# Kernel tuning notes

Measured on AMD Instinct MI355X. Metric: run time of the kernel, lower is better.

## Reference

```python
import jax, jax.numpy as jnp
import numpy as np

D_MODEL = 512
N_HEADS = 8
B, S = 4, 1024
REL_HIDDEN = 64


def setup_inputs() -> dict:
    key = jax.random.key(0)
    ks = jax.random.split(key, 16)

    def g(k, shape, scale=0.02):
        return jax.random.normal(k, shape, dtype=jnp.float32) * scale

    x = jax.random.normal(ks[0], (B, S, D_MODEL), dtype=jnp.float32)
    freqs = jax.random.uniform(ks[1], (B, S, 1), dtype=jnp.float32)
    return {
        "x": x,
        "freqs": freqs,
        "Wq": g(ks[2], (D_MODEL, D_MODEL)), "bq": g(ks[3], (D_MODEL,)),
        "Wk": g(ks[4], (D_MODEL, D_MODEL)), "bk": g(ks[5], (D_MODEL,)),
        "Wv": g(ks[6], (D_MODEL, D_MODEL)), "bv": g(ks[7], (D_MODEL,)),
        "Wo": g(ks[8], (D_MODEL, D_MODEL)), "bo": g(ks[9], (D_MODEL,)),
        "W1": g(ks[10], (2, REL_HIDDEN)), "b1": g(ks[11], (REL_HIDDEN,)),
        "W2": g(ks[12], (REL_HIDDEN, N_HEADS)), "b2": g(ks[13], (N_HEADS,)),
    }


def reference(x, freqs, Wq, bq, Wk, bk, Wv, bv, Wo, bo, W1, b1, W2, b2):
    b, s, d = x.shape
    h = N_HEADS
    dh = d // h

    def proj(W, bias):  # (b,s,d) -> (b,h,s,dh)
        return (x @ W + bias).reshape(b, s, h, dh).transpose(0, 2, 1, 3)

    Q = proj(Wq, bq)
    K = proj(Wk, bk)
    V = proj(Wv, bv)

    scores = jnp.einsum('bhid,bhjd->bhij', Q, K) / jnp.sqrt(jnp.float32(dh))

    # per-pair relative-frequency features: (b,s,s,2)
    eps = 1e-6
    fd = freqs[:, :, None, :] - freqs[:, None, :, :]
    fr = jnp.log((freqs[:, :, None, :] + eps) / (freqs[:, None, :, :] + eps))
    rel = jnp.concatenate([fd, fr], axis=-1)

    # MLP bias -> (b,s,s,h) -> (b,h,s,s)
    bias = jax.nn.relu(rel @ W1 + b1) @ W2 + b2
    scores = scores + jnp.transpose(bias, (0, 3, 1, 2))

    attn = jax.nn.softmax(scores, axis=-1)
    ctx = jnp.einsum('bhij,bhjd->bhid', attn, V)
    ctx = ctx.transpose(0, 2, 1, 3).reshape(b, s, d)
    return ctx @ Wo + bo
```

## Files before the change

### kernel.cpp

```cpp
#include <hip/hip_runtime.h>
#include <hip/hip_bf16.h>
#include <cstdint>

#define BATCH   4
#define SEQ     1024
#define DM      512
#define NH      8
#define DH      64
#define RH      64

typedef float f32x4 __attribute__((ext_vector_type(4)));
typedef __bf16 bf16x8 __attribute__((ext_vector_type(8)));

#define QB_OFF    (0)
#define KB_OFF    (4  << 20)
#define VT_OFF    (8  << 20)
#define XB_OFF    (12 << 20)
#define WT_OFF    (16 << 20)
#define WOT_OFF   (18 << 20)
#define W2T_OFF   (19 << 20)
#define AW_OFF    (20 << 20)
#define CW_OFF    (21 << 20)
#define CTXB_OFF  (22 << 20)
#define BIAS_OFF  (32 << 20)

__global__ __launch_bounds__(256) void prologue(
    const float* __restrict__ x,
    const float* __restrict__ Wq, const float* __restrict__ Wk,
    const float* __restrict__ Wv, const float* __restrict__ Wo,
    const float* __restrict__ freqs, const float* __restrict__ W1,
    const float* __restrict__ b1, const float* __restrict__ W2,
    __bf16* __restrict__ xb, __bf16* __restrict__ Wt,
    __bf16* __restrict__ Wot, float* __restrict__ Aw,
    float* __restrict__ Cw, __bf16* __restrict__ W2t)
{
    const int t = threadIdx.x;
    const int id = blockIdx.x;
    __shared__ __align__(16) float Ts[64][65];

    if (id < 1024) {
        const size_t i = ((size_t)id * 256 + t) * 8;
        const float4 a = *(const float4*)&x[i];
        const float4 b = *(const float4*)&x[i + 4];
        bf16x8 o;
        o[0] = (__bf16)a.x; o[1] = (__bf16)a.y; o[2] = (__bf16)a.z; o[3] = (__bf16)a.w;
        o[4] = (__bf16)b.x; o[5] = (__bf16)b.y; o[6] = (__bf16)b.z; o[7] = (__bf16)b.w;
        *(bf16x8*)&xb[i] = o;
    } else if (id < 1280) {
        const int lin = id - 1024;
        const int z   = lin >> 6;
        const int rem = lin & 63;
        const int k0  = (rem >> 3) * 64;
        const int n0  = (rem & 7) * 64;
        const float* __restrict__ src = (z == 0) ? Wq : (z == 1) ? Wk
                                       : (z == 2) ? Wv : Wo;
        __bf16* __restrict__ dst = (z < 3) ? (Wt + (size_t)(z * 512 + n0) * 512)
                                           : (Wot + (size_t)n0 * 512);
        #pragma unroll
        for (int i = 0; i < 4; ++i) {
            const int iid = t + i * 256;
            const int row = iid >> 4, c4 = (iid & 15) * 4;
            const float4 v = *(const float4*)&src[(size_t)(k0 + row) * DM + n0 + c4];
            Ts[row][c4 + 0] = v.x; Ts[row][c4 + 1] = v.y;
            Ts[row][c4 + 2] = v.z; Ts[row][c4 + 3] = v.w;
        }
        __syncthreads();
        #pragma unroll
        for (int i = 0; i < 2; ++i) {
            const int iid = t + i * 256;
            const int rn = iid >> 3, ck = (iid & 7) * 8;
            bf16x8 o;
            #pragma unroll
            for (int j = 0; j < 8; ++j) o[j] = (__bf16)Ts[ck + j][rn];
            *(bf16x8*)&dst[(size_t)rn * 512 + k0 + ck] = o;
        }
    } else {
        const int lin = id - 1280;
        const int row = lin * 4 + (t >> 6);
        const int k = t & 63;
        const float f = freqs[row];
        const float L = logf(f + 1e-6f);
        const float base = f * W1[k] + L * W1[RH + k];
        Aw[(size_t)row * RH + k] = base + b1[k];
        Cw[(size_t)row * RH + k] = -base;
        if (row < 16)
            W2t[row * 64 + k] = (row < NH) ? (__bf16)W2[k * NH + row] : (__bf16)0.f;
    }
}

__global__ __launch_bounds__(256) void mid_fused(
    const __bf16* __restrict__ xb, const __bf16* __restrict__ Wt,
    const float* __restrict__ bq, const float* __restrict__ bk,
    const float* __restrict__ bv,
    __bf16* __restrict__ Qb, __bf16* __restrict__ Kb, __bf16* __restrict__ Vtb,
    const float* __restrict__ Aw, const float* __restrict__ Cw,
    const __bf16* __restrict__ W2t, __bf16* __restrict__ biasb)
{
    const int t = threadIdx.x;
    __shared__ __align__(16) char smem[36864];

    if (blockIdx.x < 384) {
        const int wave = t >> 6, lane = t & 63;
        const int wm = wave >> 1, wn = wave & 1;
        const int r = lane & 15, kc = lane >> 4, q4 = kc * 4;
        const int lin = blockIdx.x;
        const int swz = (lin & 7) * 48 + (lin >> 3);
        const int m0 = (swz / 12) * 128;
        const int n0 = (swz % 12) * 128;
        const int sec = n0 >> 9;
        const int nn = n0 & 511;

        __bf16* __restrict__ As = (__bf16*)smem;
        __bf16* __restrict__ Bs = (__bf16*)(smem + 18432);

        f32x4 acc[4][4];
        #pragma unroll
        for (int i = 0; i < 4; ++i)
            #pragma unroll
            for (int j = 0; j < 4; ++j) acc[i][j] = {0.f, 0.f, 0.f, 0.f};

        const int srow = t >> 3, sck = (t & 7) * 8;
        const __bf16* __restrict__ Ag = xb + (size_t)(m0 + srow) * 512 + sck;
        const __bf16* __restrict__ Bg = Wt + (size_t)(n0 + srow) * 512 + sck;

        for (int k0 = 0; k0 < 512; k0 += 64) {
            bf16x8 ra[4], rb[4];
            #pragma unroll
            for (int i = 0; i < 4; ++i) {
                ra[i] = *(const bf16x8*)(Ag + (size_t)i * 32 * 512 + k0);
                rb[i] = *(const bf16x8*)(Bg + (size_t)i * 32 * 512 + k0);
            }
            __syncthreads();
            #pragma unroll
            for (int i = 0; i < 4; ++i) {
                *(bf16x8*)&As[(srow + i * 32) * 72 + sck] = ra[i];
                *(bf16x8*)&Bs[(srow + i * 32) * 72 + sck] = rb[i];
            }
            __syncthreads();
            #pragma unroll
            for (int ks = 0; ks < 2; ++ks) {
                bf16x8 af[4], bf[4];
                #pragma unroll
                for (int mf = 0; mf < 4; ++mf)
                    af[mf] = *(const bf16x8*)&As[(wm * 64 + mf * 16 + r) * 72 + ks * 32 + kc * 8];
                #pragma unroll
                for (int nf = 0; nf < 4; ++nf)
                    bf[nf] = *(const bf16x8*)&Bs[(wn * 64 + nf * 16 + r) * 72 + ks * 32 + kc * 8];
                #pragma unroll
                for (int mf = 0; mf < 4; ++mf)
                    #pragma unroll
                    for (int nf = 0; nf < 4; ++nf)
                        acc[mf][nf] = __builtin_amdgcn_mfma_f32_16x16x32_bf16(
                            af[mf], bf[nf], acc[mf][nf], 0, 0, 0);
            }
        }

        const float* __restrict__ bias = (sec == 0) ? bq : (sec == 1) ? bk : bv;
        __syncthreads();
        __bf16* __restrict__ Ls = (__bf16*)smem;
        if (sec < 2) {
            #pragma unroll
            for (int mf = 0; mf < 4; ++mf)
                #pragma unroll
                for (int nf = 0; nf < 4; ++nf) {
                    const int n_l = wn * 64 + nf * 16 + r;
                    const float bb = bias[nn + n_l];
                    #pragma unroll
                    for (int rr = 0; rr < 4; ++rr)
                        Ls[(wm * 64 + mf * 16 + q4 + rr) * 136 + n_l] =
                            (__bf16)(acc[mf][nf][rr] + bb);
                }
        } else {
            #pragma unroll
            for (int mf = 0; mf < 4; ++mf)
                #pragma unroll
                for (int nf = 0; nf < 4; ++nf) {
                    const int n_l = wn * 64 + nf * 16 + r;
                    const float bb = bias[nn + n_l];
                    #pragma unroll
                    for (int rr = 0; rr < 4; ++rr)
                        Ls[n_l * 136 + (wm * 64 + mf * 16 + q4 + rr)] =
                            (__bf16)(acc[mf][nf][rr] + bb);
                }
        }
        __syncthreads();

        const int b = m0 >> 10, sbase = m0 & 1023;
        if (sec < 2) {
            __bf16* __restrict__ dst = sec ? Kb : Qb;
            #pragma unroll
            for (int i = 0; i < 8; ++i) {
                const int id = t + i * 256;
                const int row = id >> 4, nc = (id & 15) * 8;
                const bf16x8 v = *(const bf16x8*)&Ls[row * 136 + nc];
                const int ng = nn + nc, h = ng >> 6, c = ng & 63;
                *(bf16x8*)&dst[((size_t)(b * NH + h) * SEQ + sbase + row) * DH + c] = v;
            }
        } else {
            #pragma unroll
            for (int i = 0; i < 8; ++i) {
                const int id = t + i * 256;
                const int nrow = id >> 4, mc = (id & 15) * 8;
                const bf16x8 v = *(const bf16x8*)&Ls[nrow * 136 + mc];
                const int ng = nn + nrow, h = ng >> 6, c = ng & 63;
                *(bf16x8*)&Vtb[((size_t)(b * NH + h) * DH + c) * SEQ + sbase + mc] = v;
            }
        }
    } else {
        const int wave = t >> 6, lane = t & 63;
        const int il = lane & 15, kc = lane >> 4;
        const int id2 = blockIdx.x - 384;
        const int b   = id2 >> 8;
        const int rem = id2 & 255;
        const int i0  = (rem >> 3) * 32;
        const int j0  = (rem & 7) * 128;

        float* __restrict__ Cs = (float*)smem;

        {
            const int jr = t >> 1, half = (t & 1) * 32;
            const float* __restrict__ src = &Cw[((size_t)b * SEQ + j0 + jr) * RH + half];
            #pragma unroll
            for (int q = 0; q < 8; ++q)
                *(float4*)&Cs[jr * 68 + half + q * 4] = *(const float4*)(src + q * 4);
        }

        const bf16x8 w2f0 = *(const bf16x8*)&W2t[il * 64 + kc * 8];
        const bf16x8 w2f1 = *(const bf16x8*)&W2t[il * 64 + 32 + kc * 8];
        __syncthreads();

        #pragma unroll
        for (int ih = 0; ih < 2; ++ih) {
            const float* __restrict__ ap =
                &Aw[((size_t)b * SEQ + i0 + ih * 16 + il) * RH];
            const float4 a0 = *(const float4*)(ap + kc * 8);
            const float4 a1 = *(const float4*)(ap + kc * 8 + 4);
            const float4 a2 = *(const float4*)(ap + 32 + kc * 8);
            const float4 a3 = *(const float4*)(ap + 32 + kc * 8 + 4);

            #pragma unroll
            for (int jb = 0; jb < 4; ++jb) {
                f32x4 accJ[8];
                #pragma unroll
                for (int jj = 0; jj < 8; ++jj) {
                    const float* __restrict__ cp =
                        &Cs[(wave * 32 + jb * 8 + jj) * 68 + kc * 8];
                    const float4 c0 = *(const float4*)(cp);
                    const float4 c1 = *(const float4*)(cp + 4);
                    const float4 c2 = *(const float4*)(cp + 32);
                    const float4 c3 = *(const float4*)(cp + 36);
                    bf16x8 hb0, hb1;
                    hb0[0] = (__bf16)fmaxf(a0.x + c0.x, 0.f);
                    hb0[1] = (__bf16)fmaxf(a0.y + c0.y, 0.f);
                    hb0[2] = (__bf16)fmaxf(a0.z + c0.z, 0.f);
                    hb0[3] = (__bf16)fmaxf(a0.w + c0.w, 0.f);
                    hb0[4] = (__bf16)fmaxf(a1.x + c1.x, 0.f);
                    hb0[5] = (__bf16)fmaxf(a1.y + c1.y, 0.f);
                    hb0[6] = (__bf16)fmaxf(a1.z + c1.z, 0.f);
                    hb0[7] = (__bf16)fmaxf(a1.w + c1.w, 0.f);
                    hb1[0] = (__bf16)fmaxf(a2.x + c2.x, 0.f);
                    hb1[1] = (__bf16)fmaxf(a2.y + c2.y, 0.f);
                    hb1[2] = (__bf16)fmaxf(a2.z + c2.z, 0.f);
                    hb1[3] = (__bf16)fmaxf(a2.w + c2.w, 0.f);
                    hb1[4] = (__bf16)fmaxf(a3.x + c3.x, 0.f);
                    hb1[5] = (__bf16)fmaxf(a3.y + c3.y, 0.f);
                    hb1[6] = (__bf16)fmaxf(a3.z + c3.z, 0.f);
                    hb1[7] = (__bf16)fmaxf(a3.w + c3.w, 0.f);
                    f32x4 acc = {0.f, 0.f, 0.f, 0.f};
                    acc = __builtin_amdgcn_mfma_f32_16x16x32_bf16(hb0, w2f0, acc, 0, 0, 0);
                    acc = __builtin_amdgcn_mfma_f32_16x16x32_bf16(hb1, w2f1, acc, 0, 0, 0);
                    accJ[jj] = acc;
                }
                if (il < 8) {
                    #pragma unroll
                    for (int rr = 0; rr < 4; ++rr) {
                        bf16x8 pv;
                        #pragma unroll
                        for (int jj = 0; jj < 8; ++jj)
                            pv[jj] = (__bf16)accJ[jj][rr];
                        *(bf16x8*)&biasb[(((size_t)b * NH + il) * SEQ
                                          + i0 + ih * 16 + kc * 4 + rr) * SEQ
                                         + j0 + wave * 32 + jb * 8] = pv;
                    }
                }
            }
        }
    }
}

#define PSTR 1032

__global__ __launch_bounds__(512) void attn_mfma(
    const __bf16* __restrict__ Qb, const __bf16* __restrict__ Kb,
    const __bf16* __restrict__ Vtb, const __bf16* __restrict__ biasb,
    __bf16* __restrict__ ctxb)
{
    const int t = threadIdx.x;
    const int wave = t >> 6, lane = t & 63;
    const int r = lane & 15, kc = lane >> 4;
    const int blk = (blockIdx.x & 7) * 256 + (blockIdx.x >> 3);
    const int it = blk & 63;
    const int h  = (blk >> 6) & 7;
    const int b  = blk >> 9;
    const int s0 = it * 16;
    const int bh = b * NH + h;

    __shared__ __align__(16) __bf16 Pb[16 * PSTR];
    __shared__ __align__(16) float part[1088];
    __shared__ float red[8][16];
    __shared__ float invl[16];

    uint32_t brg[4][8];
    {
        const uint16_t* __restrict__ bb = (const uint16_t*)biasb
            + ((size_t)bh * SEQ + s0 + kc * 4) * SEQ + wave * 128 + r;
        #pragma unroll
        for (int rr = 0; rr < 4; ++rr)
            #pragma unroll
            for (int jt = 0; jt < 8; ++jt)
                brg[rr][jt] = bb[(size_t)rr * SEQ + jt * 16];
    }

    f32x4 sc[8];
    {
        const __bf16* __restrict__ Qp = Qb + ((size_t)bh * SEQ + s0) * DH;
        const __bf16* __restrict__ Kp = Kb + ((size_t)bh * SEQ + wave * 128) * DH;
        const bf16x8 qa0 = *(const bf16x8*)(Qp + r * DH + kc * 8);
        const bf16x8 qa1 = *(const bf16x8*)(Qp + r * DH + 32 + kc * 8);
        __builtin_amdgcn_s_setprio(1);
        #pragma unroll
        for (int jt = 0; jt < 8; ++jt) {
            const bf16x8 kb0 = *(const bf16x8*)(Kp + (size_t)(jt * 16 + r) * DH + kc * 8);
            const bf16x8 kb1 = *(const bf16x8*)(Kp + (size_t)(jt * 16 + r) * DH + 32 + kc * 8);
            f32x4 a = {0.f, 0.f, 0.f, 0.f};
            a = __builtin_amdgcn_mfma_f32_16x16x32_bf16(qa0, kb0, a, 0, 0, 0);
            a = __builtin_amdgcn_mfma_f32_16x16x32_bf16(qa1, kb1, a, 0, 0, 0);
            sc[jt] = a;
        }
        __builtin_amdgcn_s_setprio(0);
    }

    float psum[4] = {0.f, 0.f, 0.f, 0.f};
    #pragma unroll
    for (int jt = 0; jt < 8; ++jt) {
        #pragma unroll
        for (int rr = 0; rr < 4; ++rr) {
            const float s = fmaf(sc[jt][rr], 0.125f,
                                 __uint_as_float(brg[rr][jt] << 16));
            const float p = __expf(fminf(s, 30.f));
            sc[jt][rr] = p;
            psum[rr] += p;
        }
    }
    #pragma unroll
    for (int mask = 8; mask >= 1; mask >>= 1)
        #pragma unroll
        for (int rr = 0; rr < 4; ++rr)
            psum[rr] += __shfl_xor(psum[rr], mask);
    if (r == 0) {
        #pragma unroll
        for (int rr = 0; rr < 4; ++rr) red[wave][kc * 4 + rr] = psum[rr];
    }
    #pragma unroll
    for (int jt = 0; jt < 8; ++jt)
        #pragma unroll
        for (int rr = 0; rr < 4; ++rr)
            Pb[(kc * 4 + rr) * PSTR + wave * 128 + jt * 16 + r] = (__bf16)sc[jt][rr];
    __syncthreads();

    if (t < 16) {
        float l = 0.f;
        #pragma unroll
        for (int w = 0; w < 8; ++w) l += red[w][t];
        invl[t] = 1.0f / l;
    }

    {
        const int ct = wave & 3, kh = wave >> 2;
        const __bf16* __restrict__ Vp =
            Vtb + ((size_t)bh * DH + ct * 16 + r) * SEQ + kh * 512;
        f32x4 acc = {0.f, 0.f, 0.f, 0.f};
        __builtin_amdgcn_s_setprio(1);
        #pragma unroll 4
        for (int jt = 0; jt < 16; ++jt) {
            const bf16x8 pa = *(const bf16x8*)&Pb[r * PSTR + kh * 512 + jt * 32 + kc * 8];
            const bf16x8 vb = *(const bf16x8*)(Vp + jt * 32 + kc * 8);
            acc = __builtin_amdgcn_mfma_f32_16x16x32_bf16(pa, vb, acc, 0, 0, 0);
        }
        __builtin_amdgcn_s_setprio(0);
        if (kh == 1) {
            #pragma unroll
            for (int rr = 0; rr < 4; ++rr)
                part[ct * 272 + (kc * 4 + rr) * 17 + r] = acc[rr];
        }
        __syncthreads();
        if (kh == 0) {
            #pragma unroll
            for (int rr = 0; rr < 4; ++rr) {
                const int row = kc * 4 + rr;
                const float v = (acc[rr] + part[ct * 272 + row * 17 + r]) * invl[row];
                ctxb[((size_t)(b * SEQ) + s0 + row) * DM + h * DH + ct * 16 + r] = (__bf16)v;
            }
        }
    }
}

__global__ __launch_bounds__(256) void gemm_out_mfma(
    const __bf16* __restrict__ ctxb, const __bf16* __restrict__ Wot,
    const float* __restrict__ bo, float* __restrict__ out)
{
    const int t = threadIdx.x;
    const int wave = t >> 6, lane = t & 63;
    const int wm = wave >> 1, wn = wave & 1;
    const int r = lane & 15, kc = lane >> 4, q4 = kc * 4;
    const int lin = blockIdx.y * 4 + blockIdx.x;
    const int swz = (lin & 7) * 16 + (lin >> 3);
    const int m0 = (swz / 4) * 128;
    const int n0 = (swz % 4) * 128;

    __shared__ __align__(16) char smem[36864];
    __bf16* __restrict__ As = (__bf16*)smem;
    __bf16* __restrict__ Bs = (__bf16*)(smem + 18432);

    f32x4 acc[4][4];
    #pragma unroll
    for (int i = 0; i < 4; ++i)
        #pragma unroll
        for (int j = 0; j < 4; ++j) acc[i][j] = {0.f, 0.f, 0.f, 0.f};

    const int srow = t >> 3, sck = (t & 7) * 8;
    const __bf16* __restrict__ Ag = ctxb + (size_t)(m0 + srow) * 512 + sck;
    const __bf16* __restrict__ Bg = Wot + (size_t)(n0 + srow) * 512 + sck;

    for (int k0 = 0; k0 < 512; k0 += 64) {
        bf16x8 ra[4], rb[4];
        #pragma unroll
        for (int i = 0; i < 4; ++i) {
            ra[i] = *(const bf16x8*)(Ag + (size_t)i * 32 * 512 + k0);
            rb[i] = *(const bf16x8*)(Bg + (size_t)i * 32 * 512 + k0);
        }
        __syncthreads();
        #pragma unroll
        for (int i = 0; i < 4; ++i) {
            *(bf16x8*)&As[(srow + i * 32) * 72 + sck] = ra[i];
            *(bf16x8*)&Bs[(srow + i * 32) * 72 + sck] = rb[i];
        }
        __syncthreads();
        #pragma unroll
        for (int ks = 0; ks < 2; ++ks) {
            bf16x8 af[4], bf[4];
            #pragma unroll
            for (int mf = 0; mf < 4; ++mf)
                af[mf] = *(const bf16x8*)&As[(wm * 64 + mf * 16 + r) * 72 + ks * 32 + kc * 8];
            #pragma unroll
            for (int nf = 0; nf < 4; ++nf)
                bf[nf] = *(const bf16x8*)&Bs[(wn * 64 + nf * 16 + r) * 72 + ks * 32 + kc * 8];
            #pragma unroll
            for (int mf = 0; mf < 4; ++mf)
                #pragma unroll
                for (int nf = 0; nf < 4; ++nf)
                    acc[mf][nf] = __builtin_amdgcn_mfma_f32_16x16x32_bf16(
                        af[mf], bf[nf], acc[mf][nf], 0, 0, 0);
        }
    }

    #pragma unroll
    for (int mf = 0; mf < 4; ++mf)
        #pragma unroll
        for (int nf = 0; nf < 4; ++nf) {
            const int n_l = wn * 64 + nf * 16 + r;
            const float bb = bo[n0 + n_l];
            #pragma unroll
            for (int rr = 0; rr < 4; ++rr)
                out[(size_t)(m0 + wm * 64 + mf * 16 + q4 + rr) * DM + n0 + n_l] =
                    acc[mf][nf][rr] + bb;
        }
}

extern "C" void kernel_launch(void* const* d_in, const int* in_sizes, int n_in,
                              void* d_out, int out_size, void* d_ws, size_t ws_size,
                              hipStream_t stream)
{
    const float* x     = (const float*)d_in[0];
    const float* freqs = (const float*)d_in[1];
    const float* Wq    = (const float*)d_in[2];
    const float* bq    = (const float*)d_in[3];
    const float* Wk    = (const float*)d_in[4];
    const float* bk    = (const float*)d_in[5];
    const float* Wv    = (const float*)d_in[6];
    const float* bv    = (const float*)d_in[7];
    const float* Wo    = (const float*)d_in[8];
    const float* bo    = (const float*)d_in[9];
    const float* W1    = (const float*)d_in[10];
    const float* b1    = (const float*)d_in[11];
    const float* W2    = (const float*)d_in[12];

    char* wsb = (char*)d_ws;
    __bf16* Qb    = (__bf16*)(wsb + QB_OFF);
    __bf16* Kb    = (__bf16*)(wsb + KB_OFF);
    __bf16* Vtb   = (__bf16*)(wsb + VT_OFF);
    __bf16* xb    = (__bf16*)(wsb + XB_OFF);
    __bf16* Wt    = (__bf16*)(wsb + WT_OFF);
    __bf16* Wot   = (__bf16*)(wsb + WOT_OFF);
    __bf16* W2t   = (__bf16*)(wsb + W2T_OFF);
    float*  Aw    = (float*)(wsb + AW_OFF);
    float*  Cw    = (float*)(wsb + CW_OFF);
    __bf16* ctxb  = (__bf16*)(wsb + CTXB_OFF);
    __bf16* biasb = (__bf16*)(wsb + BIAS_OFF);
    float* out = (float*)d_out;

    prologue<<<dim3(2304), 256, 0, stream>>>(
        x, Wq, Wk, Wv, Wo, freqs, W1, b1, W2, xb, Wt, Wot, Aw, Cw, W2t);
    mid_fused<<<dim3(1408), 256, 0, stream>>>(
        xb, Wt, bq, bk, bv, Qb, Kb, Vtb, Aw, Cw, W2t, biasb);
    attn_mfma<<<dim3(2048), 512, 0, stream>>>(Qb, Kb, Vtb, biasb, ctxb);
    gemm_out_mfma<<<dim3(4, 32), 256, 0, stream>>>(ctxb, Wot, bo, out);
}
```

Baseline: 207.7 us.

## Fuse prologue conversions into consumer kernels, dropping the prologue launch

```diff
diff --git a/kernel.cpp b/kernel.cpp
--- a/kernel.cpp
+++ b/kernel.cpp
@@ -15,86 +15,19 @@
 #define QB_OFF    (0)
 #define KB_OFF    (4  << 20)
 #define VT_OFF    (8  << 20)
-#define XB_OFF    (12 << 20)
-#define WT_OFF    (16 << 20)
-#define WOT_OFF   (18 << 20)
-#define W2T_OFF   (19 << 20)
-#define AW_OFF    (20 << 20)
-#define CW_OFF    (21 << 20)
-#define CTXB_OFF  (22 << 20)
+#define CTXB_OFF  (12 << 20)
 #define BIAS_OFF  (32 << 20)
 
-__global__ __launch_bounds__(256) void prologue(
+__global__ __launch_bounds__(256) void mid2(
     const float* __restrict__ x,
     const float* __restrict__ Wq, const float* __restrict__ Wk,
-    const float* __restrict__ Wv, const float* __restrict__ Wo,
+    const float* __restrict__ Wv,
+    const float* __restrict__ bq, const float* __restrict__ bk,
+    const float* __restrict__ bv,
     const float* __restrict__ freqs, const float* __restrict__ W1,
     const float* __restrict__ b1, const float* __restrict__ W2,
-    __bf16* __restrict__ xb, __bf16* __restrict__ Wt,
-    __bf16* __restrict__ Wot, float* __restrict__ Aw,
-    float* __restrict__ Cw, __bf16* __restrict__ W2t)
-{
-    const int t = threadIdx.x;
-    const int id = blockIdx.x;
-    __shared__ __align__(16) float Ts[64][65];
-
-    if (id < 1024) {
-        const size_t i = ((size_t)id * 256 + t) * 8;
-        const float4 a = *(const float4*)&x[i];
-        const float4 b = *(const float4*)&x[i + 4];
-        bf16x8 o;
-        o[0] = (__bf16)a.x; o[1] = (__bf16)a.y; o[2] = (__bf16)a.z; o[3] = (__bf16)a.w;
-        o[4] = (__bf16)b.x; o[5] = (__bf16)b.y; o[6] = (__bf16)b.z; o[7] = (__bf16)b.w;
-        *(bf16x8*)&xb[i] = o;
-    } else if (id < 1280) {
-        const int lin = id - 1024;
-        const int z   = lin >> 6;
-        const int rem = lin & 63;
-        const int k0  = (rem >> 3) * 64;
-        const int n0  = (rem & 7) * 64;
-        const float* __restrict__ src = (z == 0) ? Wq : (z == 1) ? Wk
-                                       : (z == 2) ? Wv : Wo;
-        __bf16* __restrict__ dst = (z < 3) ? (Wt + (size_t)(z * 512 + n0) * 512)
-                                           : (Wot + (size_t)n0 * 512);
-        #pragma unroll
-        for (int i = 0; i < 4; ++i) {
-            const int iid = t + i * 256;
-            const int row = iid >> 4, c4 = (iid & 15) * 4;
-            const float4 v = *(const float4*)&src[(size_t)(k0 + row) * DM + n0 + c4];
-            Ts[row][c4 + 0] = v.x; Ts[row][c4 + 1] = v.y;
-            Ts[row][c4 + 2] = v.z; Ts[row][c4 + 3] = v.w;
-        }
-        __syncthreads();
-        #pragma unroll
-        for (int i = 0; i < 2; ++i) {
-            const int iid = t + i * 256;
-            const int rn = iid >> 3, ck = (iid & 7) * 8;
-            bf16x8 o;
-            #pragma unroll
-            for (int j = 0; j < 8; ++j) o[j] = (__bf16)Ts[ck + j][rn];
-            *(bf16x8*)&dst[(size_t)rn * 512 + k0 + ck] = o;
-        }
-    } else {
-        const int lin = id - 1280;
-        const int row = lin * 4 + (t >> 6);
-        const int k = t & 63;
-        const float f = freqs[row];
-        const float L = logf(f + 1e-6f);
-        const float base = f * W1[k] + L * W1[RH + k];
-        Aw[(size_t)row * RH + k] = base + b1[k];
-        Cw[(size_t)row * RH + k] = -base;
-        if (row < 16)
-            W2t[row * 64 + k] = (row < NH) ? (__bf16)W2[k * NH + row] : (__bf16)0.f;
-    }
-}
-
-__global__ __launch_bounds__(256) void mid_fused(
-    const __bf16* __restrict__ xb, const __bf16* __restrict__ Wt,
-    const float* __restrict__ bq, const float* __restrict__ bk,
-    const float* __restrict__ bv,
     __bf16* __restrict__ Qb, __bf16* __restrict__ Kb, __bf16* __restrict__ Vtb,
-    const float* __restrict__ Aw, const float* __restrict__ Cw,
-    const __bf16* __restrict__ W2t, __bf16* __restrict__ biasb)
+    __bf16* __restrict__ biasb)
 {
     const int t = threadIdx.x;
     __shared__ __align__(16) char smem[36864];
@@ -109,6 +42,7 @@
         const int n0 = (swz % 12) * 128;
         const int sec = n0 >> 9;
         const int nn = n0 & 511;
+        const float* __restrict__ W = (sec == 0) ? Wq : (sec == 1) ? Wk : Wv;
 
         __bf16* __restrict__ As = (__bf16*)smem;
         __bf16* __restrict__ Bs = (__bf16*)(smem + 18432);
@@ -120,21 +54,37 @@
             for (int j = 0; j < 4; ++j) acc[i][j] = {0.f, 0.f, 0.f, 0.f};
 
         const int srow = t >> 3, sck = (t & 7) * 8;
-        const __bf16* __restrict__ Ag = xb + (size_t)(m0 + srow) * 512 + sck;
-        const __bf16* __restrict__ Bg = Wt + (size_t)(n0 + srow) * 512 + sck;
+        const int kr = t >> 2, seg = (t & 3) * 32;
 
         for (int k0 = 0; k0 < 512; k0 += 64) {
-            bf16x8 ra[4], rb[4];
+            float4 xa[4][2];
             #pragma unroll
             for (int i = 0; i < 4; ++i) {
-                ra[i] = *(const bf16x8*)(Ag + (size_t)i * 32 * 512 + k0);
-                rb[i] = *(const bf16x8*)(Bg + (size_t)i * 32 * 512 + k0);
-            }
+                const float* __restrict__ ap =
+                    &x[(size_t)(m0 + srow + i * 32) * 512 + k0 + sck];
+                xa[i][0] = *(const float4*)(ap);
+                xa[i][1] = *(const float4*)(ap + 4);
+            }
+            float4 wv[8];
+            #pragma unroll
+            for (int q = 0; q < 8; ++q)
+                wv[q] = *(const float4*)&W[(size_t)(k0 + kr) * 512 + nn + seg + q * 4];
             __syncthreads();
             #pragma unroll
             for (int i = 0; i < 4; ++i) {
-                *(bf16x8*)&As[(srow + i * 32) * 72 + sck] = ra[i];
-                *(bf16x8*)&Bs[(srow + i * 32) * 72 + sck] = rb[i];
+                bf16x8 o;
+                o[0] = (__bf16)xa[i][0].x; o[1] = (__bf16)xa[i][0].y;
+                o[2] = (__bf16)xa[i][0].z; o[3] = (__bf16)xa[i][0].w;
+                o[4] = (__bf16)xa[i][1].x; o[5] = (__bf16)xa[i][1].y;
+                o[6] = (__bf16)xa[i][1].z; o[7] = (__bf16)xa[i][1].w;
+                *(bf16x8*)&As[(srow + i * 32) * 72 + sck] = o;
+            }
+            #pragma unroll
+            for (int q = 0; q < 8; ++q) {
+                Bs[(seg + q * 4 + 0) * 72 + kr] = (__bf16)wv[q].x;
+                Bs[(seg + q * 4 + 1) * 72 + kr] = (__bf16)wv[q].y;
+                Bs[(seg + q * 4 + 2) * 72 + kr] = (__bf16)wv[q].z;
+                Bs[(seg + q * 4 + 3) * 72 + kr] = (__bf16)wv[q].w;
             }
             __syncthreads();
             #pragma unroll
@@ -219,24 +169,64 @@
 
         {
             const int jr = t >> 1, half = (t & 1) * 32;
-            const float* __restrict__ src = &Cw[((size_t)b * SEQ + j0 + jr) * RH + half];
-            #pragma unroll
-            for (int q = 0; q < 8; ++q)
-                *(float4*)&Cs[jr * 68 + half + q * 4] = *(const float4*)(src + q * 4);
-        }
-
-        const bf16x8 w2f0 = *(const bf16x8*)&W2t[il * 64 + kc * 8];
-        const bf16x8 w2f1 = *(const bf16x8*)&W2t[il * 64 + 32 + kc * 8];
+            const float fj = freqs[(size_t)b * SEQ + j0 + jr];
+            const float Lj = logf(fj + 1e-6f);
+            #pragma unroll
+            for (int q = 0; q < 8; ++q) {
+                const float4 wa = *(const float4*)&W1[half + q * 4];
+                const float4 wb = *(const float4*)&W1[64 + half + q * 4];
+                float4 cv;
+                cv.x = -(fj * wa.x + Lj * wb.x);
+                cv.y = -(fj * wa.y + Lj * wb.y);
+                cv.z = -(fj * wa.z + Lj * wb.z);
+                cv.w = -(fj * wa.w + Lj * wb.w);
+                *(float4*)&Cs[jr * 68 + half + q * 4] = cv;
+            }
+        }
+
+        bf16x8 w2f0, w2f1;
+        #pragma unroll
+        for (int m = 0; m < 8; ++m) {
+            w2f0[m] = (il < 8) ? (__bf16)W2[(kc * 8 + m) * NH + il] : (__bf16)0.f;
+            w2f1[m] = (il < 8) ? (__bf16)W2[(32 + kc * 8 + m) * NH + il] : (__bf16)0.f;
+        }
         __syncthreads();
 
         #pragma unroll
         for (int ih = 0; ih < 2; ++ih) {
-            const float* __restrict__ ap =
-                &Aw[((size_t)b * SEQ + i0 + ih * 16 + il) * RH];
-            const float4 a0 = *(const float4*)(ap + kc * 8);
-            const float4 a1 = *(const float4*)(ap + kc * 8 + 4);
-            const float4 a2 = *(const float4*)(ap + 32 + kc * 8);
-            const float4 a3 = *(const float4*)(ap + 32 + kc * 8 + 4);
+            const float fi = freqs[(size_t)b * SEQ + i0 + ih * 16 + il];
+            const float Li = logf(fi + 1e-6f);
+            float4 a0, a1, a2, a3;
+            {
+                const float4 wa0 = *(const float4*)&W1[kc * 8];
+                const float4 wb0 = *(const float4*)&W1[64 + kc * 8];
+                const float4 bb0 = *(const float4*)&b1[kc * 8];
+                a0.x = fi * wa0.x + Li * wb0.x + bb0.x;
+                a0.y = fi * wa0.y + Li * wb0.y + bb0.y;
+                a0.z = fi * wa0.z + Li * wb0.z + bb0.z;
+                a0.w = fi * wa0.w + Li * wb0.w + bb0.w;
+                const float4 wa1 = *(const float4*)&W1[kc * 8 + 4];
+                const float4 wb1 = *(const float4*)&W1[64 + kc * 8 + 4];
+                const float4 bb1 = *(const float4*)&b1[kc * 8 + 4];
+                a1.x = fi * wa1.x + Li * wb1.x + bb1.x;
+                a1.y = fi * wa1.y + Li * wb1.y + bb1.y;
+                a1.z = fi * wa1.z + Li * wb1.z + bb1.z;
+                a1.w = fi * wa1.w + Li * wb1.w + bb1.w;
+                const float4 wa2 = *(const float4*)&W1[32 + kc * 8];
+                const float4 wb2 = *(const float4*)&W1[96 + kc * 8];
+                const float4 bb2 = *(const float4*)&b1[32 + kc * 8];
+                a2.x = fi * wa2.x + Li * wb2.x + bb2.x;
+                a2.y = fi * wa2.y + Li * wb2.y + bb2.y;
+                a2.z = fi * wa2.z + Li * wb2.z + bb2.z;
+                a2.w = fi * wa2.w + Li * wb2.w + bb2.w;
+                const float4 wa3 = *(const float4*)&W1[32 + kc * 8 + 4];
+                const float4 wb3 = *(const float4*)&W1[96 + kc * 8 + 4];
+                const float4 bb3 = *(const float4*)&b1[32 + kc * 8 + 4];
+                a3.x = fi * wa3.x + Li * wb3.x + bb3.x;
+                a3.y = fi * wa3.y + Li * wb3.y + bb3.y;
+                a3.z = fi * wa3.z + Li * wb3.z + bb3.z;
+                a3.w = fi * wa3.w + Li * wb3.w + bb3.w;
+            }
 
             #pragma unroll
             for (int jb = 0; jb < 4; ++jb) {
@@ -406,7 +396,7 @@
 }
 
 __global__ __launch_bounds__(256) void gemm_out_mfma(
-    const __bf16* __restrict__ ctxb, const __bf16* __restrict__ Wot,
+    const __bf16* __restrict__ ctxb, const float* __restrict__ Wo,
     const float* __restrict__ bo, float* __restrict__ out)
 {
     const int t = threadIdx.x;
@@ -429,21 +419,28 @@
         for (int j = 0; j < 4; ++j) acc[i][j] = {0.f, 0.f, 0.f, 0.f};
 
     const int srow = t >> 3, sck = (t & 7) * 8;
+    const int kr = t >> 2, seg = (t & 3) * 32;
     const __bf16* __restrict__ Ag = ctxb + (size_t)(m0 + srow) * 512 + sck;
-    const __bf16* __restrict__ Bg = Wot + (size_t)(n0 + srow) * 512 + sck;
 
     for (int k0 = 0; k0 < 512; k0 += 64) {
-        bf16x8 ra[4], rb[4];
-        #pragma unroll
-        for (int i = 0; i < 4; ++i) {
+        bf16x8 ra[4];
+        #pragma unroll
+        for (int i = 0; i < 4; ++i)
             ra[i] = *(const bf16x8*)(Ag + (size_t)i * 32 * 512 + k0);
-            rb[i] = *(const bf16x8*)(Bg + (size_t)i * 32 * 512 + k0);
-        }
+        float4 wv[8];
+        #pragma unroll
+        for (int q = 0; q < 8; ++q)
+            wv[q] = *(const float4*)&Wo[(size_t)(k0 + kr) * 512 + n0 + seg + q * 4];
         __syncthreads();
         #pragma unroll
-        for (int i = 0; i < 4; ++i) {
+        for (int i = 0; i < 4; ++i)
             *(bf16x8*)&As[(srow + i * 32) * 72 + sck] = ra[i];
-            *(bf16x8*)&Bs[(srow + i * 32) * 72 + sck] = rb[i];
+        #pragma unroll
+        for (int q = 0; q < 8; ++q) {
+            Bs[(seg + q * 4 + 0) * 72 + kr] = (__bf16)wv[q].x;
+            Bs[(seg + q * 4 + 1) * 72 + kr] = (__bf16)wv[q].y;
+            Bs[(seg + q * 4 + 2) * 72 + kr] = (__bf16)wv[q].z;
+            Bs[(seg + q * 4 + 3) * 72 + kr] = (__bf16)wv[q].w;
         }
         __syncthreads();
         #pragma unroll
@@ -499,20 +496,12 @@
     __bf16* Qb    = (__bf16*)(wsb + QB_OFF);
     __bf16* Kb    = (__bf16*)(wsb + KB_OFF);
     __bf16* Vtb   = (__bf16*)(wsb + VT_OFF);
-    __bf16* xb    = (__bf16*)(wsb + XB_OFF);
-    __bf16* Wt    = (__bf16*)(wsb + WT_OFF);
-    __bf16* Wot   = (__bf16*)(wsb + WOT_OFF);
-    __bf16* W2t   = (__bf16*)(wsb + W2T_OFF);
-    float*  Aw    = (float*)(wsb + AW_OFF);
-    float*  Cw    = (float*)(wsb + CW_OFF);
     __bf16* ctxb  = (__bf16*)(wsb + CTXB_OFF);
     __bf16* biasb = (__bf16*)(wsb + BIAS_OFF);
     float* out = (float*)d_out;
 
-    prologue<<<dim3(2304), 256, 0, stream>>>(
-        x, Wq, Wk, Wv, Wo, freqs, W1, b1, W2, xb, Wt, Wot, Aw, Cw, W2t);
-    mid_fused<<<dim3(1408), 256, 0, stream>>>(
-        xb, Wt, bq, bk, bv, Qb, Kb, Vtb, Aw, Cw, W2t, biasb);
+    mid2<<<dim3(1408), 256, 0, stream>>>(
+        x, Wq, Wk, Wv, bq, bk, bv, freqs, W1, b1, W2, Qb, Kb, Vtb, biasb);
     attn_mfma<<<dim3(2048), 512, 0, stream>>>(Qb, Kb, Vtb, biasb, ctxb);
-    gemm_out_mfma<<<dim3(4, 32), 256, 0, stream>>>(ctxb, Wot, bo, out);
+    gemm_out_mfma<<<dim3(4, 32), 256, 0, stream>>>(ctxb, Wo, bo, out);
 }
```

Result: slower. 227.2 us (+9.4%).

## Store relative-position bias in MFMA-fragment-native layout for vectorized attention loads

Applied to the files above, without the earlier changes.

```diff
diff --git a/kernel.cpp b/kernel.cpp
--- a/kernel.cpp
+++ b/kernel.cpp
@@ -213,7 +213,8 @@
         const int b   = id2 >> 8;
         const int rem = id2 & 255;
         const int i0  = (rem >> 3) * 32;
-        const int j0  = (rem & 7) * 128;
+        const int j0w = rem & 7;
+        const int j0  = j0w * 128;
 
         float* __restrict__ Cs = (float*)smem;
 
@@ -237,6 +238,12 @@
             const float4 a1 = *(const float4*)(ap + kc * 8 + 4);
             const float4 a2 = *(const float4*)(ap + 32 + kc * 8);
             const float4 a3 = *(const float4*)(ap + 32 + kc * 8 + 4);
+
+            const int qt = (i0 >> 4) + ih;
+            __bf16* __restrict__ bout = (il < 8)
+                ? (biasb + (((size_t)(b * NH + il) * 64 + qt) * 16384)
+                   + (size_t)j0w * 4096)
+                : nullptr;
 
             #pragma unroll
             for (int jb = 0; jb < 4; ++jb) {
@@ -273,14 +280,13 @@
                 }
                 if (il < 8) {
                     #pragma unroll
-                    for (int rr = 0; rr < 4; ++rr) {
-                        bf16x8 pv;
+                    for (int jj = 0; jj < 8; ++jj) {
+                        const int within = wave * 32 + jb * 8 + jj;
+                        const int jt_a = within >> 4, r_a = within & 15;
                         #pragma unroll
-                        for (int jj = 0; jj < 8; ++jj)
-                            pv[jj] = (__bf16)accJ[jj][rr];
-                        *(bf16x8*)&biasb[(((size_t)b * NH + il) * SEQ
-                                          + i0 + ih * 16 + kc * 4 + rr) * SEQ
-                                         + j0 + wave * 32 + jb * 8] = pv;
+                        for (int rr = 0; rr < 4; ++rr)
+                            bout[(kc * 16 + r_a) * 32 + rr * 8 + jt_a] =
+                                (__bf16)accJ[jj][rr];
                     }
                 }
             }
@@ -310,15 +316,14 @@
     __shared__ float red[8][16];
     __shared__ float invl[16];
 
-    uint32_t brg[4][8];
+    bf16x8 brg8[4];
     {
-        const uint16_t* __restrict__ bb = (const uint16_t*)biasb
-            + ((size_t)bh * SEQ + s0 + kc * 4) * SEQ + wave * 128 + r;
-        #pragma unroll
-        for (int rr = 0; rr < 4; ++rr)
-            #pragma unroll
-            for (int jt = 0; jt < 8; ++jt)
-                brg[rr][jt] = bb[(size_t)rr * SEQ + jt * 16];
+        const __bf16* __restrict__ bb = biasb
+            + (((size_t)bh * 64 + it) * 16384)
+            + (size_t)wave * 4096 + (kc * 16 + r) * 32;
+        #pragma unroll
+        for (int q = 0; q < 4; ++q)
+            brg8[q] = *(const bf16x8*)(bb + q * 8);
     }
 
     f32x4 sc[8];
@@ -345,8 +350,7 @@
     for (int jt = 0; jt < 8; ++jt) {
         #pragma unroll
         for (int rr = 0; rr < 4; ++rr) {
-            const float s = fmaf(sc[jt][rr], 0.125f,
-                                 __uint_as_float(brg[rr][jt] << 16));
+            const float s = fmaf(sc[jt][rr], 0.125f, (float)brg8[rr][jt]);
             const float p = __expf(fminf(s, 30.f));
             sc[jt][rr] = p;
             psum[rr] += p;
```

Measured after the change: 323.1 us. 55.5% more time.
